# Optimization experiments

Hardware: AMD Instinct MI355X
Metric: run time of the kernel (lower is better)

The kernel has to match this reference:

```python
import jax, jax.numpy as jnp
import numpy as np

B, T, H, U = 32, 2048, 1024, 1024

def setup_inputs() -> dict:
    key = jax.random.key(0)
    ks = jax.random.split(key, 8)
    s = 1.0 / np.sqrt(H)
    return {
        "dec_hidden": jax.random.normal(ks[0], (B, H), jnp.float32),
        "all_enc_hiddens": jax.random.normal(ks[1], (B, T, H), jnp.float32),
        "W1": jax.random.normal(ks[2], (H, U), jnp.float32) * s,
        "b1": jnp.zeros((U,), jnp.float32),
        "W2": jax.random.normal(ks[3], (H, U), jnp.float32) * s,
        "b2": jnp.zeros((U,), jnp.float32),
        "V": jax.random.normal(ks[4], (U, 1), jnp.float32) * (1.0 / np.sqrt(U)),
        "bv": jnp.zeros((1,), jnp.float32),
    }

def reference(dec_hidden, all_enc_hiddens, W1, b1, W2, b2, V, bv):
    # query projection: [B, 1, U]
    q = (dec_hidden @ W1 + b1)[:, None, :]
    # key projection: [B, T, U]
    k = jnp.einsum("bth,hu->btu", all_enc_hiddens, W2) + b2
    # additive score: [B, T, 1]
    score = jnp.tanh(q + k) @ V + bv
    # softmax over time axis
    attn = jax.nn.softmax(score, axis=1)  # [B, T, 1]
    # weighted context: [B, H]
    context = jnp.sum(attn * all_enc_hiddens, axis=1)
    return (context, attn)
```

## Files before the change

kernel.cpp:

```cpp
#include <hip/hip_runtime.h>
#include <hip/hip_bf16.h>
#include <math.h>

#define B_SZ 32
#define T_SZ 2048
#define H_SZ 1024
#define U_SZ 1024

#define BM 64
#define BN 256
#define BK 64
#define UT_N (U_SZ / BN)
#define BM2 256

typedef __attribute__((ext_vector_type(8))) short bf16x8;
typedef __attribute__((ext_vector_type(4))) float f32x4;

__device__ __forceinline__ unsigned int f2bf(float f) {
  union { float f; unsigned int u; } x; x.f = f;
  unsigned int r = x.u + 0x7FFFu + ((x.u >> 16) & 1u);
  return r >> 16;
}

__device__ __forceinline__ float bf2f(unsigned int lo16) {
  union { unsigned int u; float f; } x; x.u = lo16 << 16; return x.f;
}

__device__ __forceinline__ void async_cp16(const unsigned short* g, unsigned short* l) {
  __builtin_amdgcn_global_load_lds(
      (const __attribute__((address_space(1))) unsigned int*)g,
      (__attribute__((address_space(3))) unsigned int*)l, 16, 0, 0);
}

__device__ __forceinline__ float fast_tanh(float x) {
  const float e = __expf(x + x);
  return (e - 1.0f) * __builtin_amdgcn_rcpf(e + 1.0f);
}

__global__ __launch_bounds__(256) void k_prep(
    const float* __restrict__ enc, unsigned short* __restrict__ encb,
    const float* __restrict__ W2, unsigned short* __restrict__ W2t,
    const float* __restrict__ dec, const float* __restrict__ W1,
    const float* __restrict__ b1, const float* __restrict__ b2,
    float* __restrict__ qq, int cvtN)
{
  __shared__ char lds_raw[64 * 65 * 2];
  const int bid = blockIdx.x;
  const int tid = threadIdx.x;

  if (bid < cvtN) {
    const size_t i = ((size_t)bid * 256 + tid) * 8;
    const float4 a = *(const float4*)(enc + i);
    const float4 b = *(const float4*)(enc + i + 4);
    uint4 o;
    o.x = f2bf(a.x) | (f2bf(a.y) << 16);
    o.y = f2bf(a.z) | (f2bf(a.w) << 16);
    o.z = f2bf(b.x) | (f2bf(b.y) << 16);
    o.w = f2bf(b.z) | (f2bf(b.w) << 16);
    *(uint4*)(encb + i) = o;
  } else if (bid < cvtN + 256) {
    unsigned short (*tile)[65] = (unsigned short(*)[65])lds_raw;
    const int idx = bid - cvtN;
    const int bu = idx & 15, bh = idx >> 4;
    const int tc = tid & 63, tr = tid >> 6;
    #pragma unroll
    for (int i = 0; i < 16; ++i) {
      const int hl = tr + i * 4;
      tile[tc][hl] = (unsigned short)f2bf(W2[(size_t)(bh * 64 + hl) * U_SZ + bu * 64 + tc]);
    }
    __syncthreads();
    #pragma unroll
    for (int i = 0; i < 16; ++i) {
      const int ul = tr + i * 4;
      W2t[(size_t)(bu * 64 + ul) * H_SZ + bh * 64 + tc] = tile[ul][tc];
    }
  } else {
    float (*red)[64] = (float(*)[64])lds_raw;
    const int idx = bid - (cvtN + 256);
    const int ul = tid & 63;
    const int hq = tid >> 6;
    const int u  = (idx & 15) * 64 + ul;
    const int b  = idx >> 4;
    const float* dh = dec + b * H_SZ + hq * 256;
    const float* w  = W1 + (size_t)(hq * 256) * U_SZ + u;
    float acc = 0.0f;
    #pragma unroll 8
    for (int h = 0; h < 256; ++h) acc += dh[h] * w[(size_t)h * U_SZ];
    red[hq][ul] = acc;
    __syncthreads();
    if (tid < 64) {
      const float s = red[0][ul] + red[1][ul] + red[2][ul] + red[3][ul];
      qq[b * U_SZ + u] = s + b1[u] + b2[u];
    }
  }
}

__global__ __launch_bounds__(512, 2) void k_gemm_score2(
    const unsigned short* __restrict__ encb,
    const unsigned short* __restrict__ W2t,
    const float* __restrict__ qq, const float* __restrict__ Vv,
    float* __restrict__ score)
{
  __shared__ unsigned short Al[2][BM2 * BK];
  __shared__ unsigned short Bl[2][BN * BK];

  const int tid  = threadIdx.x;
  const int wid  = tid >> 6;
  const int lane = tid & 63;
  const int quad = lane >> 4;
  const int l16  = lane & 15;
  const int wr   = wid >> 2;
  const int wc   = wid & 3;
  const int m0   = blockIdx.x * BM2;
  const int b    = m0 >> 11;

  unsigned int aoff[4], boff[4];
  int swi[4];
  #pragma unroll
  for (int j = 0; j < 4; ++j) {
    const int sw = j * 8 + wid;
    const int s  = sw * 64 + lane;
    const int r  = s >> 3;
    const int c  = ((s & 7) - r) & 7;
    aoff[j] = (unsigned int)((m0 + r) * H_SZ + c * 8);
    boff[j] = (unsigned int)(r * H_SZ + c * 8);
    swi[j]  = sw * 512;
  }

  f32x4 acc[8][4];
  float part[8][4];
  #pragma unroll
  for (int rt = 0; rt < 8; ++rt)
    #pragma unroll
    for (int ct = 0; ct < 4; ++ct) {
      part[rt][ct] = 0.0f;
      #pragma unroll
      for (int r = 0; r < 4; ++r) acc[rt][ct][r] = 0.0f;
    }

  auto STAGE = [&](int i) {
    const int ut = i >> 4;
    const unsigned int kk = (unsigned int)(i & 15) * 64u;
    const int bs = i & 1;
    #pragma unroll
    for (int j = 0; j < 4; ++j)
      async_cp16(encb + aoff[j] + kk, &Al[bs][swi[j]]);
    const unsigned int uoff = (unsigned int)(ut * 256) * H_SZ + kk;
    #pragma unroll
    for (int j = 0; j < 4; ++j)
      async_cp16(W2t + uoff + boff[j], &Bl[bs][swi[j]]);
  };

  auto COMPUTE = [&](int i) {
    const unsigned short* Ab = Al[i & 1];
    const unsigned short* Bb = Bl[i & 1];
    #pragma unroll
    for (int h = 0; h < 2; ++h) {
      bf16x8 af[8], bfr[4];
      #pragma unroll
      for (int rt = 0; rt < 8; ++rt) {
        const int ar = wr * 128 + rt * 16 + l16;
        af[rt] = *(const bf16x8*)&Ab[ar * 64 + ((h * 4 + quad + ar) & 7) * 8];
      }
      #pragma unroll
      for (int ct = 0; ct < 4; ++ct) {
        const int bu = wc * 64 + ct * 16 + l16;
        bfr[ct] = *(const bf16x8*)&Bb[bu * 64 + ((h * 4 + quad + bu) & 7) * 8];
      }
      #pragma unroll
      for (int rt = 0; rt < 8; ++rt)
        #pragma unroll
        for (int ct = 0; ct < 4; ++ct)
          acc[rt][ct] = __builtin_amdgcn_mfma_f32_16x16x32_bf16(
              af[rt], bfr[ct], acc[rt][ct], 0, 0, 0);
    }
  };

  auto EPILOGUE = [&](int ut) {
    #pragma unroll
    for (int ct = 0; ct < 4; ++ct) {
      const int u = ut * 256 + wc * 64 + ct * 16 + l16;
      const float qv = qq[b * U_SZ + u];
      const float vv = Vv[u];
      #pragma unroll
      for (int rt = 0; rt < 8; ++rt)
        #pragma unroll
        for (int r = 0; r < 4; ++r)
          part[rt][r] += fast_tanh(acc[rt][ct][r] + qv) * vv;
    }
    #pragma unroll
    for (int rt = 0; rt < 8; ++rt)
      #pragma unroll
      for (int ct = 0; ct < 4; ++ct)
        #pragma unroll
        for (int r = 0; r < 4; ++r) acc[rt][ct][r] = 0.0f;
  };

  STAGE(0);
  for (int i = 0; i < 63; ++i) {
    STAGE(i + 1);
    asm volatile("s_waitcnt vmcnt(8)" ::: "memory");
    __builtin_amdgcn_s_barrier();
    __builtin_amdgcn_sched_barrier(0);
    COMPUTE(i);
    if ((i & 15) == 15) EPILOGUE(i >> 4);
    __builtin_amdgcn_sched_barrier(0);
    __builtin_amdgcn_s_barrier();
  }
  asm volatile("s_waitcnt vmcnt(0)" ::: "memory");
  __builtin_amdgcn_s_barrier();
  __builtin_amdgcn_sched_barrier(0);
  COMPUTE(63);
  EPILOGUE(3);

  __syncthreads();
  float* scoreS = (float*)&Al[0][0];
  if (tid < BM2) scoreS[tid] = 0.0f;
  __syncthreads();
  #pragma unroll
  for (int rt = 0; rt < 8; ++rt)
    #pragma unroll
    for (int r = 0; r < 4; ++r) {
      float p = part[rt][r];
      p += __shfl_xor(p, 1);
      p += __shfl_xor(p, 2);
      p += __shfl_xor(p, 4);
      p += __shfl_xor(p, 8);
      if (l16 == 0) atomicAdd(&scoreS[wr * 128 + rt * 16 + quad * 4 + r], p);
    }
  __syncthreads();
  if (tid < BM2) score[m0 + tid] = scoreS[tid];
}

__global__ __launch_bounds__(256) void k_gemm_score_f32(
    const float* __restrict__ encf,
    const unsigned short* __restrict__ W2t,
    const float* __restrict__ qq, const float* __restrict__ Vv,
    float* __restrict__ score)
{
  __shared__ unsigned short Alo[BM * BK];
  __shared__ unsigned short Blo[BN * BK];
  __shared__ float scoreS[BM];

  const int tid  = threadIdx.x;
  const int wave = tid >> 6;
  const int lane = tid & 63;
  const int quad = lane >> 4;
  const int l16  = lane & 15;
  const int m0   = blockIdx.x * BM;
  const int b    = m0 >> 11;

  if (tid < BM) scoreS[tid] = 0.0f;

  size_t boff[8]; unsigned short* dstB[8];
  #pragma unroll
  for (int i = 0; i < 8; ++i) {
    const int slot = (i * 4 + wave) * 64 + lane;
    const int r = slot >> 3;
    const int c = ((slot & 7) - r) & 7;
    boff[i] = (size_t)r * H_SZ + c * 8;
    dstB[i] = &Blo[(i * 4 + wave) * 512];
  }

  const int ar[4] = { 0 * 16 + l16, 1 * 16 + l16, 2 * 16 + l16, 3 * 16 + l16 };
  const int bu[4] = { wave * 64 + 0 * 16 + l16, wave * 64 + 1 * 16 + l16,
                      wave * 64 + 2 * 16 + l16, wave * 64 + 3 * 16 + l16 };

  for (int ut = 0; ut < UT_N; ++ut) {
    const int u0 = ut * BN;
    f32x4 acc[4][4];
    #pragma unroll
    for (int rt = 0; rt < 4; ++rt)
      #pragma unroll
      for (int ct = 0; ct < 4; ++ct)
        #pragma unroll
        for (int r = 0; r < 4; ++r) acc[rt][ct][r] = 0.0f;

    for (int kk = 0; kk < H_SZ; kk += BK) {
      __syncthreads();
      #pragma unroll
      for (int i = 0; i < 2; ++i) {
        const int slot = i * 256 + tid;
        const int r = slot >> 3;
        const int c = ((slot & 7) - r) & 7;
        const float* src = encf + (size_t)(m0 + r) * H_SZ + kk + c * 8;
        const float4 x = *(const float4*)src;
        const float4 y = *(const float4*)(src + 4);
        uint4 o;
        o.x = f2bf(x.x) | (f2bf(x.y) << 16);
        o.y = f2bf(x.z) | (f2bf(x.w) << 16);
        o.z = f2bf(y.x) | (f2bf(y.y) << 16);
        o.w = f2bf(y.z) | (f2bf(y.w) << 16);
        *(uint4*)&Alo[slot * 8] = o;
      }
      #pragma unroll
      for (int i = 0; i < 8; ++i)
        async_cp16(W2t + (size_t)u0 * H_SZ + boff[i] + kk, dstB[i]);
      __syncthreads();

      #pragma unroll
      for (int h = 0; h < 2; ++h) {
        bf16x8 af[4], bfr[4];
        #pragma unroll
        for (int rt = 0; rt < 4; ++rt)
          af[rt] = *(const bf16x8*)&Alo[ar[rt] * 64 + ((h * 4 + quad + ar[rt]) & 7) * 8];
        #pragma unroll
        for (int ct = 0; ct < 4; ++ct)
          bfr[ct] = *(const bf16x8*)&Blo[bu[ct] * 64 + ((h * 4 + quad + bu[ct]) & 7) * 8];
        #pragma unroll
        for (int rt = 0; rt < 4; ++rt)
          #pragma unroll
          for (int ct = 0; ct < 4; ++ct)
            acc[rt][ct] = __builtin_amdgcn_mfma_f32_16x16x32_bf16(
                af[rt], bfr[ct], acc[rt][ct], 0, 0, 0);
      }
    }

    float part[4][4];
    #pragma unroll
    for (int rt = 0; rt < 4; ++rt)
      #pragma unroll
      for (int r = 0; r < 4; ++r) part[rt][r] = 0.0f;
    #pragma unroll
    for (int ct = 0; ct < 4; ++ct) {
      const int u = u0 + wave * 64 + ct * 16 + l16;
      const float qv = qq[b * U_SZ + u];
      const float vv = Vv[u];
      #pragma unroll
      for (int rt = 0; rt < 4; ++rt)
        #pragma unroll
        for (int r = 0; r < 4; ++r)
          part[rt][r] += fast_tanh(acc[rt][ct][r] + qv) * vv;
    }
    #pragma unroll
    for (int rt = 0; rt < 4; ++rt)
      #pragma unroll
      for (int r = 0; r < 4; ++r) {
        float p = part[rt][r];
        p += __shfl_xor(p, 1);
        p += __shfl_xor(p, 2);
        p += __shfl_xor(p, 4);
        p += __shfl_xor(p, 8);
        part[rt][r] = p;
      }
    if (l16 == 0) {
      #pragma unroll
      for (int rt = 0; rt < 4; ++rt)
        #pragma unroll
        for (int r = 0; r < 4; ++r)
          atomicAdd(&scoreS[rt * 16 + quad * 4 + r], part[rt][r]);
    }
  }
  __syncthreads();
  if (tid < BM) score[m0 + tid] = scoreS[tid];
}

__global__ void k_softmax(const float* __restrict__ score, float* __restrict__ attn) {
  const int b = blockIdx.x;
  const int tid = threadIdx.x;
  __shared__ float wmax[4], wsum[4];
  const float* s = score + b * T_SZ;
  float v[8];
  float lmax = -INFINITY;
  #pragma unroll
  for (int i = 0; i < 8; ++i) { v[i] = s[tid + i * 256]; lmax = fmaxf(lmax, v[i]); }
  #pragma unroll
  for (int m = 1; m <= 32; m <<= 1) lmax = fmaxf(lmax, __shfl_xor(lmax, m));
  if ((tid & 63) == 0) wmax[tid >> 6] = lmax;
  __syncthreads();
  const float gmax = fmaxf(fmaxf(wmax[0], wmax[1]), fmaxf(wmax[2], wmax[3]));
  float lsum = 0.0f;
  #pragma unroll
  for (int i = 0; i < 8; ++i) { v[i] = __expf(v[i] - gmax); lsum += v[i]; }
  #pragma unroll
  for (int m = 1; m <= 32; m <<= 1) lsum += __shfl_xor(lsum, m);
  if ((tid & 63) == 0) wsum[tid >> 6] = lsum;
  __syncthreads();
  const float inv = 1.0f / (wsum[0] + wsum[1] + wsum[2] + wsum[3]);
  #pragma unroll
  for (int i = 0; i < 8; ++i) attn[b * T_SZ + tid + i * 256] = v[i] * inv;
}

__global__ void k_context_bf16(const unsigned short* __restrict__ encb,
                               const float* __restrict__ attn, float* __restrict__ ctx) {
  const int tcx = blockIdx.x;
  const int hc  = blockIdx.y;
  const int b   = blockIdx.z;
  const int h0  = hc * 512 + threadIdx.x * 2;
  const unsigned short* e = encb + ((size_t)b * T_SZ + tcx * 256) * H_SZ + h0;
  const float* a = attn + b * T_SZ + tcx * 256;
  float c0 = 0, c1 = 0;
  #pragma unroll 4
  for (int t = 0; t < 256; ++t) {
    const unsigned int v = *(const unsigned int*)&e[(size_t)t * H_SZ];
    c0 += a[t] * bf2f(v & 0xFFFFu);
    c1 += a[t] * bf2f(v >> 16);
  }
  atomicAdd(&ctx[b * H_SZ + h0],     c0);
  atomicAdd(&ctx[b * H_SZ + h0 + 1], c1);
}

__global__ void k_context_f32(const float* __restrict__ enc,
                              const float* __restrict__ attn, float* __restrict__ ctx) {
  const int tcx = blockIdx.x, hc = blockIdx.y, b = blockIdx.z;
  const int h = hc * 256 + threadIdx.x;
  const float* e = enc + ((size_t)b * T_SZ + tcx * 256) * H_SZ + h;
  const float* a = attn + b * T_SZ + tcx * 256;
  float a0 = 0, a1 = 0, a2 = 0, a3 = 0;
  for (int t = 0; t < 256; t += 4) {
    a0 += a[t]     * e[(size_t)t * H_SZ];
    a1 += a[t + 1] * e[(size_t)(t + 1) * H_SZ];
    a2 += a[t + 2] * e[(size_t)(t + 2) * H_SZ];
    a3 += a[t + 3] * e[(size_t)(t + 3) * H_SZ];
  }
  atomicAdd(&ctx[b * H_SZ + h], (a0 + a1) + (a2 + a3));
}

extern "C" void kernel_launch(void* const* d_in, const int* in_sizes, int n_in,
                              void* d_out, int out_size, void* d_ws, size_t ws_size,
                              hipStream_t stream) {
  const float* dec = (const float*)d_in[0];
  const float* enc = (const float*)d_in[1];
  const float* W1  = (const float*)d_in[2];
  const float* b1  = (const float*)d_in[3];
  const float* W2  = (const float*)d_in[4];
  const float* b2  = (const float*)d_in[5];
  const float* Vv  = (const float*)d_in[6];

  const size_t encb_bytes = (size_t)B_SZ * T_SZ * H_SZ * 2;
  const size_t fast_need  = encb_bytes + (2u << 20) + (128u << 10) + (256u << 10);
  const bool fast = ws_size >= fast_need;

  char* ws = (char*)d_ws;
  unsigned short* encb = nullptr;
  unsigned short* W2t;
  float *qq, *score;
  if (fast) {
    encb  = (unsigned short*)ws;
    W2t   = (unsigned short*)(ws + encb_bytes);
    qq    = (float*)(ws + encb_bytes + (2u << 20));
    score = (float*)(ws + encb_bytes + (2u << 20) + (128u << 10));
  } else {
    W2t   = (unsigned short*)ws;
    qq    = (float*)(ws + (2u << 20));
    score = (float*)(ws + (2u << 20) + (128u << 10));
  }

  float* ctx  = (float*)d_out;
  float* attn = (float*)d_out + B_SZ * H_SZ;

  hipMemsetAsync(ctx, 0, B_SZ * H_SZ * sizeof(float), stream);
  const int cvtN = fast ? (B_SZ * T_SZ * H_SZ) / (256 * 8) : 0;
  k_prep<<<cvtN + 256 + 512, 256, 0, stream>>>(enc, encb, W2, W2t,
                                               dec, W1, b1, b2, qq, cvtN);
  if (fast)
    k_gemm_score2<<<(B_SZ * T_SZ) / BM2, 512, 0, stream>>>(encb, W2t, qq, Vv, score);
  else
    k_gemm_score_f32<<<(B_SZ * T_SZ) / BM, 256, 0, stream>>>(enc, W2t, qq, Vv, score);
  k_softmax<<<32, 256, 0, stream>>>(score, attn);
  if (fast)
    k_context_bf16<<<dim3(8, 2, 32), 256, 0, stream>>>(encb, attn, ctx);
  else
    k_context_f32<<<dim3(8, 4, 32), 256, 0, stream>>>(enc, attn, ctx);
}
```

Baseline: 599.4 us.

## Interleave GEMM prefetch with split MFMA phases and fuse softmax into context

```diff
diff --git a/kernel.cpp b/kernel.cpp
--- a/kernel.cpp
+++ b/kernel.cpp
@@ -138,80 +138,117 @@
       for (int r = 0; r < 4; ++r) acc[rt][ct][r] = 0.0f;
     }
 
-  auto STAGE = [&](int i) {
-    const int ut = i >> 4;
-    const unsigned int kk = (unsigned int)(i & 15) * 64u;
-    const int bs = i & 1;
-    #pragma unroll
-    for (int j = 0; j < 4; ++j)
-      async_cp16(encb + aoff[j] + kk, &Al[bs][swi[j]]);
-    const unsigned int uoff = (unsigned int)(ut * 256) * H_SZ + kk;
-    #pragma unroll
-    for (int j = 0; j < 4; ++j)
-      async_cp16(W2t + uoff + boff[j], &Bl[bs][swi[j]]);
+  float qv[4], vv[4];
+  bf16x8 af[4], bfr[4];
+
+  auto STAGE_A = [&](int t, int j) {
+    async_cp16(encb + aoff[j] + (unsigned int)(t & 15) * 64u, &Al[t & 1][swi[j]]);
   };
-
-  auto COMPUTE = [&](int i) {
+  auto STAGE_B = [&](int t, int j) {
+    const unsigned int uo = (unsigned int)((t >> 4) * 256) * H_SZ
+                          + (unsigned int)(t & 15) * 64u;
+    async_cp16(W2t + uo + boff[j], &Bl[t & 1][swi[j]]);
+  };
+  auto LDA = [&](const unsigned short* Ab, int rtB, int h) {
+    #pragma unroll
+    for (int k = 0; k < 4; ++k) {
+      const int ar = wr * 128 + (rtB + k) * 16 + l16;
+      af[k] = *(const bf16x8*)&Ab[ar * 64 + ((h * 4 + quad + ar) & 7) * 8];
+    }
+  };
+  auto LDB = [&](const unsigned short* Bb, int h) {
+    #pragma unroll
+    for (int ct = 0; ct < 4; ++ct) {
+      const int bu = wc * 64 + ct * 16 + l16;
+      bfr[ct] = *(const bf16x8*)&Bb[bu * 64 + ((h * 4 + quad + bu) & 7) * 8];
+    }
+  };
+  auto MFMA16 = [&](int rtB) {
+    #pragma unroll
+    for (int k = 0; k < 4; ++k)
+      #pragma unroll
+      for (int ct = 0; ct < 4; ++ct)
+        acc[rtB + k][ct] = __builtin_amdgcn_mfma_f32_16x16x32_bf16(
+            af[k], bfr[ct], acc[rtB + k][ct], 0, 0, 0);
+  };
+
+  #pragma unroll
+  for (int j = 0; j < 4; ++j) STAGE_A(0, j);
+  #pragma unroll
+  for (int j = 0; j < 4; ++j) STAGE_B(0, j);
+
+  #pragma unroll 2
+  for (int i = 0; i < 64; ++i) {
     const unsigned short* Ab = Al[i & 1];
     const unsigned short* Bb = Bl[i & 1];
-    #pragma unroll
-    for (int h = 0; h < 2; ++h) {
-      bf16x8 af[8], bfr[4];
-      #pragma unroll
-      for (int rt = 0; rt < 8; ++rt) {
-        const int ar = wr * 128 + rt * 16 + l16;
-        af[rt] = *(const bf16x8*)&Ab[ar * 64 + ((h * 4 + quad + ar) & 7) * 8];
-      }
-      #pragma unroll
-      for (int ct = 0; ct < 4; ++ct) {
-        const int bu = wc * 64 + ct * 16 + l16;
-        bfr[ct] = *(const bf16x8*)&Bb[bu * 64 + ((h * 4 + quad + bu) & 7) * 8];
-      }
-      #pragma unroll
-      for (int rt = 0; rt < 8; ++rt)
-        #pragma unroll
-        for (int ct = 0; ct < 4; ++ct)
-          acc[rt][ct] = __builtin_amdgcn_mfma_f32_16x16x32_bf16(
-              af[rt], bfr[ct], acc[rt][ct], 0, 0, 0);
-    }
-  };
-
-  auto EPILOGUE = [&](int ut) {
-    #pragma unroll
-    for (int ct = 0; ct < 4; ++ct) {
-      const int u = ut * 256 + wc * 64 + ct * 16 + l16;
-      const float qv = qq[b * U_SZ + u];
-      const float vv = Vv[u];
-      #pragma unroll
-      for (int rt = 0; rt < 8; ++rt)
-        #pragma unroll
-        for (int r = 0; r < 4; ++r)
-          part[rt][r] += fast_tanh(acc[rt][ct][r] + qv) * vv;
-    }
-    #pragma unroll
-    for (int rt = 0; rt < 8; ++rt)
-      #pragma unroll
-      for (int ct = 0; ct < 4; ++ct)
-        #pragma unroll
-        for (int r = 0; r < 4; ++r) acc[rt][ct][r] = 0.0f;
-  };
-
-  STAGE(0);
-  for (int i = 0; i < 63; ++i) {
-    STAGE(i + 1);
-    asm volatile("s_waitcnt vmcnt(8)" ::: "memory");
+    const bool pf = (i < 63);
+
+    asm volatile("s_waitcnt vmcnt(0)" ::: "memory");
     __builtin_amdgcn_s_barrier();
     __builtin_amdgcn_sched_barrier(0);
-    COMPUTE(i);
-    if ((i & 15) == 15) EPILOGUE(i >> 4);
+
+    if ((i & 15) == 0) {
+      const int u0 = (i >> 4) * 256;
+      #pragma unroll
+      for (int ct = 0; ct < 4; ++ct) {
+        const int u = u0 + wc * 64 + ct * 16 + l16;
+        qv[ct] = qq[b * U_SZ + u];
+        vv[ct] = Vv[u];
+      }
+    }
+
+    LDB(Bb, 0);
+    LDA(Ab, 0, 0);
+    if (pf) { STAGE_A(i + 1, 0); STAGE_A(i + 1, 1); STAGE_A(i + 1, 2); }
+    asm volatile("s_waitcnt lgkmcnt(0)" ::: "memory");
     __builtin_amdgcn_sched_barrier(0);
+    __builtin_amdgcn_s_setprio(1);
+    MFMA16(0);
+    __builtin_amdgcn_s_setprio(0);
     __builtin_amdgcn_s_barrier();
-  }
-  asm volatile("s_waitcnt vmcnt(0)" ::: "memory");
-  __builtin_amdgcn_s_barrier();
-  __builtin_amdgcn_sched_barrier(0);
-  COMPUTE(63);
-  EPILOGUE(3);
+
+    LDA(Ab, 4, 0);
+    if (pf) { STAGE_A(i + 1, 3); STAGE_B(i + 1, 0); STAGE_B(i + 1, 1); }
+    asm volatile("s_waitcnt lgkmcnt(0)" ::: "memory");
+    __builtin_amdgcn_sched_barrier(0);
+    __builtin_amdgcn_s_setprio(1);
+    MFMA16(4);
+    __builtin_amdgcn_s_setprio(0);
+    __builtin_amdgcn_s_barrier();
+
+    LDB(Bb, 1);
+    LDA(Ab, 0, 1);
+    if (pf) { STAGE_B(i + 1, 2); STAGE_B(i + 1, 3); }
+    asm volatile("s_waitcnt lgkmcnt(0)" ::: "memory");
+    __builtin_amdgcn_sched_barrier(0);
+    __builtin_amdgcn_s_setprio(1);
+    MFMA16(0);
+    __builtin_amdgcn_s_setprio(0);
+    __builtin_amdgcn_s_barrier();
+
+    LDA(Ab, 4, 1);
+    asm volatile("s_waitcnt lgkmcnt(0)" ::: "memory");
+    __builtin_amdgcn_sched_barrier(0);
+    __builtin_amdgcn_s_setprio(1);
+    MFMA16(4);
+    __builtin_amdgcn_s_setprio(0);
+
+    if ((i & 15) == 15) {
+      #pragma unroll
+      for (int ct = 0; ct < 4; ++ct)
+        #pragma unroll
+        for (int rt = 0; rt < 8; ++rt)
+          #pragma unroll
+          for (int r = 0; r < 4; ++r)
+            part[rt][r] += fast_tanh(acc[rt][ct][r] + qv[ct]) * vv[ct];
+      #pragma unroll
+      for (int rt = 0; rt < 8; ++rt)
+        #pragma unroll
+        for (int ct = 0; ct < 4; ++ct)
+          #pragma unroll
+          for (int r = 0; r < 4; ++r) acc[rt][ct][r] = 0.0f;
+    }
+  }
 
   __syncthreads();
   float* scoreS = (float*)&Al[0][0];
@@ -324,13 +361,13 @@
     #pragma unroll
     for (int ct = 0; ct < 4; ++ct) {
       const int u = u0 + wave * 64 + ct * 16 + l16;
-      const float qv = qq[b * U_SZ + u];
-      const float vv = Vv[u];
+      const float qvs = qq[b * U_SZ + u];
+      const float vvs = Vv[u];
       #pragma unroll
       for (int rt = 0; rt < 4; ++rt)
         #pragma unroll
         for (int r = 0; r < 4; ++r)
-          part[rt][r] += fast_tanh(acc[rt][ct][r] + qv) * vv;
+          part[rt][r] += fast_tanh(acc[rt][ct][r] + qvs) * vvs;
     }
     #pragma unroll
     for (int rt = 0; rt < 4; ++rt)
@@ -381,20 +418,50 @@
   for (int i = 0; i < 8; ++i) attn[b * T_SZ + tid + i * 256] = v[i] * inv;
 }
 
-__global__ void k_context_bf16(const unsigned short* __restrict__ encb,
-                               const float* __restrict__ attn, float* __restrict__ ctx) {
+__global__ __launch_bounds__(256) void k_ctx_sm(
+    const unsigned short* __restrict__ encb,
+    const float* __restrict__ score,
+    float* __restrict__ attn, float* __restrict__ ctx)
+{
   const int tcx = blockIdx.x;
   const int hc  = blockIdx.y;
   const int b   = blockIdx.z;
-  const int h0  = hc * 512 + threadIdx.x * 2;
+  const int tid = threadIdx.x;
+  __shared__ float wmax[4], wsum[4];
+  __shared__ float att_l[256];
+
+  const float* s = score + b * T_SZ;
+  float v[8];
+  float lmax = -INFINITY;
+  #pragma unroll
+  for (int i = 0; i < 8; ++i) { v[i] = s[tid + i * 256]; lmax = fmaxf(lmax, v[i]); }
+  #pragma unroll
+  for (int m = 1; m <= 32; m <<= 1) lmax = fmaxf(lmax, __shfl_xor(lmax, m));
+  if ((tid & 63) == 0) wmax[tid >> 6] = lmax;
+  __syncthreads();
+  const float gmax = fmaxf(fmaxf(wmax[0], wmax[1]), fmaxf(wmax[2], wmax[3]));
+  float lsum = 0.0f;
+  #pragma unroll
+  for (int i = 0; i < 8; ++i) { v[i] = __expf(v[i] - gmax); lsum += v[i]; }
+  #pragma unroll
+  for (int m = 1; m <= 32; m <<= 1) lsum += __shfl_xor(lsum, m);
+  if ((tid & 63) == 0) wsum[tid >> 6] = lsum;
+  __syncthreads();
+  const float inv = 1.0f / (wsum[0] + wsum[1] + wsum[2] + wsum[3]);
+
+  const float av = __expf(s[tcx * 256 + tid] - gmax) * inv;
+  att_l[tid] = av;
+  if (hc == 0) attn[b * T_SZ + tcx * 256 + tid] = av;
+  __syncthreads();
+
+  const int h0 = hc * 512 + tid * 2;
   const unsigned short* e = encb + ((size_t)b * T_SZ + tcx * 256) * H_SZ + h0;
-  const float* a = attn + b * T_SZ + tcx * 256;
   float c0 = 0, c1 = 0;
   #pragma unroll 4
   for (int t = 0; t < 256; ++t) {
-    const unsigned int v = *(const unsigned int*)&e[(size_t)t * H_SZ];
-    c0 += a[t] * bf2f(v & 0xFFFFu);
-    c1 += a[t] * bf2f(v >> 16);
+    const unsigned int w = *(const unsigned int*)&e[(size_t)t * H_SZ];
+    c0 += att_l[t] * bf2f(w & 0xFFFFu);
+    c1 += att_l[t] * bf2f(w >> 16);
   }
   atomicAdd(&ctx[b * H_SZ + h0],     c0);
   atomicAdd(&ctx[b * H_SZ + h0 + 1], c1);
@@ -453,13 +520,12 @@
   const int cvtN = fast ? (B_SZ * T_SZ * H_SZ) / (256 * 8) : 0;
   k_prep<<<cvtN + 256 + 512, 256, 0, stream>>>(enc, encb, W2, W2t,
                                                dec, W1, b1, b2, qq, cvtN);
-  if (fast)
+  if (fast) {
     k_gemm_score2<<<(B_SZ * T_SZ) / BM2, 512, 0, stream>>>(encb, W2t, qq, Vv, score);
-  else
+    k_ctx_sm<<<dim3(8, 2, 32), 256, 0, stream>>>(encb, score, attn, ctx);
+  } else {
     k_gemm_score_f32<<<(B_SZ * T_SZ) / BM, 256, 0, stream>>>(enc, W2t, qq, Vv, score);
-  k_softmax<<<32, 256, 0, stream>>>(score, attn);
-  if (fast)
-    k_context_bf16<<<dim3(8, 2, 32), 256, 0, stream>>>(encb, attn, ctx);
-  else
+    k_softmax<<<32, 256, 0, stream>>>(score, attn);
     k_context_f32<<<dim3(8, 4, 32), 256, 0, stream>>>(enc, attn, ctx);
-}
+  }
+}
```

Result: slower. 625.0 us (+4.3%).
